# Optimization experiments

Hardware: AMD Instinct MI355X
Metric: run time of the kernel (lower is better)

The kernel has to match this reference:

```python
import jax, jax.numpy as jnp
import numpy as np

B, M, IN, HID, A = 4096, 64, 3, 128, 64
D = 50.0                       # waveguide_bound
H_CONST = 5.0
PMAX = 10.0 ** (30 / 10 - 3)   # = 1.0 (30 dBm in Watts)
C_LIGHT = 3.0e8
FC = 6.0e9
DELTA_MIN = (C_LIGHT / FC) / 2.0  # 0.025
ALPHA = 0.2                    # LeakyReLU slope


def setup_inputs() -> dict:
    key = jax.random.key(0)
    ks = jax.random.split(key, 9)
    s = lambda k, sh: (jax.random.normal(k, sh, jnp.float32) * 0.1)
    return {
        "users": jax.random.normal(ks[0], (B, M, IN), jnp.float32),
        "W1": s(ks[1], (IN, HID)),    # GAT layer 1 projection (applied as h @ W)
        "a1": s(ks[2], (2 * HID,)),   # GAT layer 1 attention vector
        "W2": s(ks[3], (HID, HID)),   # GAT layer 2 projection
        "a2": s(ks[4], (2 * HID,)),
        "mw1": s(ks[5], (HID, 32)),   # MLP Linear(hidden, 32)
        "mb1": jnp.zeros((32,), jnp.float32),
        "mw2": s(ks[6], (32, 2 * A)), # MLP Linear(32, 2*num_antennas)
        "mb2": jnp.zeros((2 * A,), jnp.float32),
    }


def gat_layer(h, W, a):
    # Wh: [B, M, d]
    Wh = h @ W
    d = W.shape[1]
    # e[b,i,j] = leakyrelu( cat(Wh_i, Wh_j) . a ) = leakyrelu( Wh_i.a[:d] + Wh_j.a[d:] )
    si = Wh @ a[:d]          # [B, M]
    sj = Wh @ a[d:]          # [B, M]
    e = jax.nn.leaky_relu(si[:, :, None] + sj[:, None, :], ALPHA)  # [B, M, M]
    attn = jax.nn.softmax(e, axis=-1)  # softmax over neighbors j (dropout p=0 -> identity)
    h_prime = jnp.einsum('bij,bjd->bid', attn, Wh)
    return jax.nn.elu(h_prime)


def reference(users, W1, a1, W2, a2, mw1, mb1, mw2, mb2):
    h = gat_layer(users, W1, a1)
    h = gat_layer(h, W2, a2)
    pooled = jnp.max(h, axis=1)                      # [B, hidden]
    readout = jax.nn.relu(pooled @ mw1 + mb1) @ mw2 + mb2  # [B, 2A]
    raw_delta, raw_power = readout[:, :A], readout[:, A:]
    eps = 1e-6
    raw_delta = jax.nn.relu(raw_delta) + eps
    raw_power = jax.nn.relu(raw_power) + eps
    Bmax = 2.0 * D - (A - 1) * DELTA_MIN
    delta = Bmax * raw_delta / (jnp.sum(raw_delta, axis=1, keepdims=True) + eps)
    power = PMAX * raw_power / (jnp.sum(raw_power, axis=1, keepdims=True) + eps)
    return power, delta
```

## Files before the change

kernel.cpp:

```cpp
#include <hip/hip_runtime.h>

#define NBATCH 4096
#define OUT2 (NBATCH * 64)

typedef _Float16 f16;
typedef __attribute__((ext_vector_type(8))) _Float16 f16x8;
typedef __attribute__((ext_vector_type(4))) float f32x4;

__device__ __forceinline__ float lrelu(float x) { return fmaxf(x, 0.2f * x); }
__device__ __forceinline__ float elu1(float x)  { return x > 0.0f ? x : __expf(x) - 1.0f; }
__device__ __forceinline__ void lds_fence() {
    asm volatile("s_waitcnt lgkmcnt(0)" ::: "memory");
}
__device__ __forceinline__ unsigned pk2(float a, float b) {
    union { f16 h[2]; unsigned u; } t;
    t.h[0] = (f16)a; t.h[1] = (f16)b;
    return t.u;
}
__device__ __forceinline__ f16x8 xpose(unsigned p0l, unsigned p0h,
                                       unsigned p1l, unsigned p1h,
                                       int s0, int s1, bool hiSel) {
    const unsigned a0l = (unsigned)__shfl((int)p0l, s0, 64);
    const unsigned a0h = (unsigned)__shfl((int)p0h, s0, 64);
    const unsigned b0l = (unsigned)__shfl((int)p0l, s1, 64);
    const unsigned b0h = (unsigned)__shfl((int)p0h, s1, 64);
    const unsigned a1l = (unsigned)__shfl((int)p1l, s0, 64);
    const unsigned a1h = (unsigned)__shfl((int)p1h, s0, 64);
    const unsigned b1l = (unsigned)__shfl((int)p1l, s1, 64);
    const unsigned b1h = (unsigned)__shfl((int)p1h, s1, 64);
    union { unsigned u[4]; f16x8 v; } o;
    o.u[0] = hiSel ? a1l : a0l;
    o.u[1] = hiSel ? a1h : a0h;
    o.u[2] = hiSel ? b1l : b0l;
    o.u[3] = hiSel ? b1h : b0h;
    return o.v;
}

__global__ void prep(const float* __restrict__ W2, const float* __restrict__ W1,
                     const float* __restrict__ a1, const float* __restrict__ a2,
                     f16* __restrict__ w2b, float* __restrict__ w1a, f16* __restrict__ w2ab) {
    const int flat = blockIdx.x * 256 + threadIdx.x;
    const int slot = flat >> 3, j = flat & 7;
    const int F2T = slot >> 8, kf = (slot >> 6) & 3, ln = slot & 63;
    const int lq = ln >> 4, lr = ln & 15;
    w2b[flat] = (f16)W2[(kf * 32 + lq * 8 + j) * 128 + F2T * 16 + lr];
    if (flat < 2048) {
        const int ks = flat >> 9, ln2 = (flat >> 3) & 63, jj = flat & 7;
        const int k = ks * 32 + ((ln2 >> 4) & 3) * 8 + jj;
        const int n = ln2 & 15;
        float v = 0.f;
        if (n < 2) {
            const float* av = a2 + n * 128;
            for (int f2 = 0; f2 < 128; ++f2) v = fmaf(W2[k * 128 + f2], av[f2], v);
        }
        w2ab[flat] = (f16)v;
    }
    if (flat >= 16381) {
        const int c = flat - 16381;
        float si = 0.f, sj = 0.f;
        for (int f = 0; f < 128; ++f) {
            const float w = W1[c * 128 + f];
            si = fmaf(w, a1[f], si);
            sj = fmaf(w, a1[128 + f], sj);
        }
        w1a[c] = si; w1a[3 + c] = sj;
    }
}

__global__ __launch_bounds__(256, 2)
void gat_kernel(const float* __restrict__ users,
                const float* __restrict__ W1,
                const f16* __restrict__ w2b,
                const float* __restrict__ w1a,
                const f16* __restrict__ w2ab,
                const float* __restrict__ mw1,
                const float* __restrict__ mb1,
                const float* __restrict__ mw2,
                const float* __restrict__ mb2,
                float* __restrict__ out)
{
    const int wid  = threadIdx.x >> 6;
    const int b    = blockIdx.x * 4 + wid;
    const int lane = threadIdx.x & 63;
    const int lr   = lane & 15;
    const int lq   = lane >> 4;
    const int s0   = (lane & 15) | ((lane & 16) << 1);
    const int s1   = s0 + 16;
    const bool hiSel = (lane & 32) != 0;

    __shared__ __align__(16) char smem[4 * 1280];
    char*  sw    = smem + wid * 1280;
    float* sSi   = (float*)(sw);
    float* sSj   = (float*)(sw + 256);
    float* sPool = (float*)(sw + 512);
    float* sHid  = (float*)(sw + 1024);

    const float* u = users + b * 192;

    {
        const float x = u[lane * 3], y = u[lane * 3 + 1], z = u[lane * 3 + 2];
        sSi[lane] = fmaf(x, w1a[0], fmaf(y, w1a[1], z * w1a[2]));
        sSj[lane] = fmaf(x, w1a[3], fmaf(y, w1a[4], z * w1a[5]));
    }
    lds_fence();

    f16x8 bfr[4];
    {
        float sjv[16];
        *(float4*)&sjv[0]  = *(const float4*)&sSj[lq * 8];
        *(float4*)&sjv[4]  = *(const float4*)&sSj[lq * 8 + 4];
        *(float4*)&sjv[8]  = *(const float4*)&sSj[32 + lq * 8];
        *(float4*)&sjv[12] = *(const float4*)&sSj[32 + lq * 8 + 4];
        f16x8 ap[4][2];
        #pragma unroll
        for (int mt = 0; mt < 4; ++mt) {
            const float si = sSi[mt * 16 + lr];
            float pv[16];
            float lsum = 0.f;
            #pragma unroll
            for (int jj = 0; jj < 8; ++jj) {
                const float p0 = __expf(lrelu(si + sjv[jj]));
                const float p1 = __expf(lrelu(si + sjv[8 + jj]));
                pv[jj] = p0; pv[8 + jj] = p1;
                lsum += p0 + p1;
            }
            lsum += __shfl_xor(lsum, 16, 64);
            lsum += __shfl_xor(lsum, 32, 64);
            const float inv = 1.0f / lsum;
            #pragma unroll
            for (int jj = 0; jj < 8; ++jj) {
                ap[mt][0][jj] = (f16)(pv[jj] * inv);
                ap[mt][1][jj] = (f16)(pv[8 + jj] * inv);
            }
        }
        f16x8 af2[2];
        #pragma unroll
        for (int ks = 0; ks < 2; ++ks) {
            #pragma unroll
            for (int jj = 0; jj < 8; ++jj) {
                const int node = ks * 32 + lq * 8 + jj;
                af2[ks][jj] = (lr < 3) ? (f16)u[node * 3 + lr] : (f16)0.f;
            }
        }
        #pragma unroll
        for (int nt = 0; nt < 4; ++nt) {
            f32x4 d1 = (f32x4){0.f, 0.f, 0.f, 0.f};
            d1 = __builtin_amdgcn_mfma_f32_16x16x32_f16(af2[0], ap[nt][0], d1, 0, 0, 0);
            d1 = __builtin_amdgcn_mfma_f32_16x16x32_f16(af2[1], ap[nt][1], d1, 0, 0, 0);
            const float c0 = __shfl(d1[0], lr, 64);
            const float c1 = __shfl(d1[1], lr, 64);
            const float c2 = __shfl(d1[2], lr, 64);
            #pragma unroll
            for (int jj = 0; jj < 8; ++jj) bfr[nt][jj] = (f16)0.f;
            if (lq == 0) {
                bfr[nt][0] = (f16)c0; bfr[nt][1] = (f16)c1; bfr[nt][2] = (f16)c2;
            }
        }
    }

    f16x8 hf[4][4];
    #pragma unroll
    for (int h = 0; h < 2; ++h) {
        #pragma unroll
        for (int ksl = 0; ksl < 2; ++ksl) {
            f32x4 acc[4][2];
            #pragma unroll
            for (int tp = 0; tp < 2; ++tp) {
                const int ftl = 2 * ksl + tp;
                f16x8 af3;
                #pragma unroll
                for (int jj = 0; jj < 8; ++jj) af3[jj] = (f16)0.f;
                if (lq == 0) {
                    #pragma unroll
                    for (int jj = 0; jj < 3; ++jj)
                        af3[jj] = (f16)W1[jj * 128 + (h * 4 + ftl) * 16 + lr];
                }
                #pragma unroll
                for (int nt = 0; nt < 4; ++nt) {
                    acc[nt][tp] = (f32x4){0.f, 0.f, 0.f, 0.f};
                    acc[nt][tp] = __builtin_amdgcn_mfma_f32_16x16x32_f16(af3, bfr[nt], acc[nt][tp], 0, 0, 0);
                }
            }
            #pragma unroll
            for (int nt = 0; nt < 4; ++nt) {
                const unsigned p0l = pk2(elu1(acc[nt][0][0]), elu1(acc[nt][0][1]));
                const unsigned p0h = pk2(elu1(acc[nt][0][2]), elu1(acc[nt][0][3]));
                const unsigned p1l = pk2(elu1(acc[nt][1][0]), elu1(acc[nt][1][1]));
                const unsigned p1h = pk2(elu1(acc[nt][1][2]), elu1(acc[nt][1][3]));
                hf[nt][h * 2 + ksl] = xpose(p0l, p0h, p1l, p1h, s0, s1, hiSel);
            }
        }
    }

    {
        f32x4 sacc[4];
        #pragma unroll
        for (int mt = 0; mt < 4; ++mt) sacc[mt] = (f32x4){0.f, 0.f, 0.f, 0.f};
        #pragma unroll
        for (int ks = 0; ks < 4; ++ks) {
            f16x8 bsw = *(const f16x8*)(w2ab + (ks * 64 + lane) * 8);
            #pragma unroll
            for (int mt = 0; mt < 4; ++mt)
                sacc[mt] = __builtin_amdgcn_mfma_f32_16x16x32_f16(hf[mt][ks], bsw, sacc[mt], 0, 0, 0);
        }
        lds_fence();
        if (lr < 2) {
            float* dst = (lr == 0) ? sSi : sSj;
            #pragma unroll
            for (int mt = 0; mt < 4; ++mt)
                #pragma unroll
                for (int r = 0; r < 4; ++r)
                    dst[mt * 16 + lq * 4 + r] = sacc[mt][r];
        }
    }
    lds_fence();

    f16x8 bp[4][2];
    {
        float sjv[16];
        *(float4*)&sjv[0]  = *(const float4*)&sSj[lq * 8];
        *(float4*)&sjv[4]  = *(const float4*)&sSj[lq * 8 + 4];
        *(float4*)&sjv[8]  = *(const float4*)&sSj[32 + lq * 8];
        *(float4*)&sjv[12] = *(const float4*)&sSj[32 + lq * 8 + 4];
        #pragma unroll
        for (int mt = 0; mt < 4; ++mt) {
            const float si = sSi[mt * 16 + lr];
            float pv[16];
            float lsum = 0.f;
            #pragma unroll
            for (int jj = 0; jj < 8; ++jj) {
                const float p0 = __expf(lrelu(si + sjv[jj]));
                const float p1 = __expf(lrelu(si + sjv[8 + jj]));
                pv[jj] = p0; pv[8 + jj] = p1;
                lsum += p0 + p1;
            }
            lsum += __shfl_xor(lsum, 16, 64);
            lsum += __shfl_xor(lsum, 32, 64);
            const float inv = 1.0f / lsum;
            #pragma unroll
            for (int jj = 0; jj < 8; ++jj) {
                bp[mt][0][jj] = (f16)(pv[jj] * inv);
                bp[mt][1][jj] = (f16)(pv[8 + jj] * inv);
            }
        }
    }

    #pragma unroll
    for (int ft = 0; ft < 8; ++ft) {
        f16x8 bw2[4];
        #pragma unroll
        for (int kf = 0; kf < 4; ++kf)
            bw2[kf] = *(const f16x8*)(w2b + ((ft * 4 + kf) * 64 + lane) * 8);
        unsigned pkq[4][2];
        #pragma unroll
        for (int nt = 0; nt < 4; ++nt) {
            f32x4 acc = (f32x4){0.f, 0.f, 0.f, 0.f};
            #pragma unroll
            for (int kf = 0; kf < 4; ++kf)
                acc = __builtin_amdgcn_mfma_f32_16x16x32_f16(hf[nt][kf], bw2[kf], acc, 0, 0, 0);
            pkq[nt][0] = pk2(acc[0], acc[1]);
            pkq[nt][1] = pk2(acc[2], acc[3]);
        }
        const f16x8 bh0 = xpose(pkq[0][0], pkq[0][1], pkq[1][0], pkq[1][1], s0, s1, hiSel);
        const f16x8 bh1 = xpose(pkq[2][0], pkq[2][1], pkq[3][0], pkq[3][1], s0, s1, hiSel);

        float mx = -1e30f;
        #pragma unroll
        for (int mt = 0; mt < 4; ++mt) {
            f32x4 acc = (f32x4){0.f, 0.f, 0.f, 0.f};
            acc = __builtin_amdgcn_mfma_f32_16x16x32_f16(bp[mt][0], bh0, acc, 0, 0, 0);
            acc = __builtin_amdgcn_mfma_f32_16x16x32_f16(bp[mt][1], bh1, acc, 0, 0, 0);
            mx = fmaxf(mx, fmaxf(fmaxf(acc[0], acc[1]), fmaxf(acc[2], acc[3])));
        }
        mx = fmaxf(mx, __shfl_xor(mx, 16, 64));
        mx = fmaxf(mx, __shfl_xor(mx, 32, 64));
        if (lane < 16) sPool[ft * 16 + lane] = elu1(mx);
    }
    lds_fence();

    {
        const int o = lane & 31, hh = lane >> 5;
        float s0r = 0.f;
        #pragma unroll 8
        for (int kk = 0; kk < 64; ++kk) {
            const int c = hh * 64 + kk;
            s0r = fmaf(sPool[c], mw1[c * 32 + o], s0r);
        }
        s0r += __shfl_xor(s0r, 32, 64);
        if (lane < 32) sHid[lane] = fmaxf(s0r + mb1[o], 0.0f);
    }
    lds_fence();
    {
        float sA = mb2[lane], sB = mb2[64 + lane];
        #pragma unroll 8
        for (int q = 0; q < 32; ++q) {
            const float wA = mw2[q * 128 + lane];
            const float wB = mw2[q * 128 + 64 + lane];
            const float h0 = sHid[q];
            sA = fmaf(h0, wA, sA);  sB = fmaf(h0, wB, sB);
        }
        float rA = fmaxf(sA, 0.0f) + 1e-6f, rB = fmaxf(sB, 0.0f) + 1e-6f;
        float uA = rA, uB = rB;
        #pragma unroll
        for (int m = 1; m < 64; m <<= 1) {
            uA += __shfl_xor(uA, m, 64);  uB += __shfl_xor(uB, m, 64);
        }
        out[b * 64 + lane]        = rB / (uB + 1e-6f);
        out[OUT2 + b * 64 + lane] = 98.425f * rA / (uA + 1e-6f);
    }
}

extern "C" void kernel_launch(void* const* d_in, const int* in_sizes, int n_in,
                              void* d_out, int out_size, void* d_ws, size_t ws_size,
                              hipStream_t stream) {
    const float* users = (const float*)d_in[0];
    const float* W1    = (const float*)d_in[1];
    const float* a1    = (const float*)d_in[2];
    const float* W2    = (const float*)d_in[3];
    const float* a2    = (const float*)d_in[4];
    const float* mw1   = (const float*)d_in[5];
    const float* mb1   = (const float*)d_in[6];
    const float* mw2   = (const float*)d_in[7];
    const float* mb2   = (const float*)d_in[8];
    float* out = (float*)d_out;

    f16*   w2b  = (f16*)d_ws;
    float* w1a  = (float*)((char*)d_ws + 32768);
    f16*   w2ab = (f16*)((char*)d_ws + 32800);

    prep<<<64, 256, 0, stream>>>(W2, W1, a1, a2, w2b, w1a, w2ab);
    gat_kernel<<<NBATCH / 4, 256, 0, stream>>>(users, W1, w2b, w1a, w2ab,
                                               mw1, mb1, mw2, mb2, out);
}
```

Before: 113.2 us.

## Stagger wave start with s_sleep, pack f16 fragments, software-pipeline W2 loads

Each wave now sleeps at launch for a number of s_sleep iterations set by its block and wave index, so that waves hit global memory and MFMA at different times. The softmax attention fragments and the layer-1 B fragments are built with packed half2 conversions instead of per-element f16 writes. The layer-2 feature-tile loop is no longer unrolled and is software-pipelined, loading the next tile's W2 fragments from global memory while the current tile's MFMAs run. The deliberate sleep adds latency to every wave, and the rolled loop may cost scheduling freedom and registers in exchange for smaller code.

```diff
diff --git a/kernel.cpp b/kernel.cpp
--- a/kernel.cpp
+++ b/kernel.cpp
@@ -17,6 +17,8 @@
     t.h[0] = (f16)a; t.h[1] = (f16)b;
     return t.u;
 }
+union F16x8U { unsigned u[4]; f16x8 v; };
+
 __device__ __forceinline__ f16x8 xpose(unsigned p0l, unsigned p0h,
                                        unsigned p1l, unsigned p1h,
                                        int s0, int s1, bool hiSel) {
@@ -28,7 +30,7 @@
     const unsigned a1h = (unsigned)__shfl((int)p1h, s0, 64);
     const unsigned b1l = (unsigned)__shfl((int)p1l, s1, 64);
     const unsigned b1h = (unsigned)__shfl((int)p1h, s1, 64);
-    union { unsigned u[4]; f16x8 v; } o;
+    F16x8U o;
     o.u[0] = hiSel ? a1l : a0l;
     o.u[1] = hiSel ? a1h : a0h;
     o.u[2] = hiSel ? b1l : b0l;
@@ -88,6 +90,11 @@
     const int s1   = s0 + 16;
     const bool hiSel = (lane & 32) != 0;
 
+    {
+        const int stg = __builtin_amdgcn_readfirstlane(((blockIdx.x >> 3) & 3) * 4 + wid);
+        for (int i = 0; i < stg; ++i) __builtin_amdgcn_s_sleep(16);
+    }
+
     __shared__ __align__(16) char smem[4 * 1280];
     char*  sw    = smem + wid * 1280;
     float* sSi   = (float*)(sw);
@@ -127,11 +134,14 @@
             lsum += __shfl_xor(lsum, 16, 64);
             lsum += __shfl_xor(lsum, 32, 64);
             const float inv = 1.0f / lsum;
-            #pragma unroll
-            for (int jj = 0; jj < 8; ++jj) {
-                ap[mt][0][jj] = (f16)(pv[jj] * inv);
-                ap[mt][1][jj] = (f16)(pv[8 + jj] * inv);
-            }
+            F16x8U a0, a1;
+            #pragma unroll
+            for (int d = 0; d < 4; ++d) {
+                a0.u[d] = pk2(pv[2 * d] * inv,     pv[2 * d + 1] * inv);
+                a1.u[d] = pk2(pv[8 + 2 * d] * inv, pv[8 + 2 * d + 1] * inv);
+            }
+            ap[mt][0] = a0.v;
+            ap[mt][1] = a1.v;
         }
         f16x8 af2[2];
         #pragma unroll
@@ -150,11 +160,11 @@
             const float c0 = __shfl(d1[0], lr, 64);
             const float c1 = __shfl(d1[1], lr, 64);
             const float c2 = __shfl(d1[2], lr, 64);
-            #pragma unroll
-            for (int jj = 0; jj < 8; ++jj) bfr[nt][jj] = (f16)0.f;
-            if (lq == 0) {
-                bfr[nt][0] = (f16)c0; bfr[nt][1] = (f16)c1; bfr[nt][2] = (f16)c2;
-            }
+            F16x8U t;
+            t.u[0] = (lq == 0) ? pk2(c0, c1)   : 0u;
+            t.u[1] = (lq == 0) ? pk2(c2, 0.0f) : 0u;
+            t.u[2] = 0u; t.u[3] = 0u;
+            bfr[nt] = t.v;
         }
     }
 
@@ -237,44 +247,62 @@
             lsum += __shfl_xor(lsum, 16, 64);
             lsum += __shfl_xor(lsum, 32, 64);
             const float inv = 1.0f / lsum;
-            #pragma unroll
-            for (int jj = 0; jj < 8; ++jj) {
-                bp[mt][0][jj] = (f16)(pv[jj] * inv);
-                bp[mt][1][jj] = (f16)(pv[8 + jj] * inv);
-            }
-        }
-    }
-
-    #pragma unroll
-    for (int ft = 0; ft < 8; ++ft) {
-        f16x8 bw2[4];
+            F16x8U b0, b1;
+            #pragma unroll
+            for (int d = 0; d < 4; ++d) {
+                b0.u[d] = pk2(pv[2 * d] * inv,     pv[2 * d + 1] * inv);
+                b1.u[d] = pk2(pv[8 + 2 * d] * inv, pv[8 + 2 * d + 1] * inv);
+            }
+            bp[mt][0] = b0.v;
+            bp[mt][1] = b1.v;
+        }
+    }
+
+    {
+        f16x8 bw2c[4];
         #pragma unroll
         for (int kf = 0; kf < 4; ++kf)
-            bw2[kf] = *(const f16x8*)(w2b + ((ft * 4 + kf) * 64 + lane) * 8);
-        unsigned pkq[4][2];
-        #pragma unroll
-        for (int nt = 0; nt < 4; ++nt) {
-            f32x4 acc = (f32x4){0.f, 0.f, 0.f, 0.f};
-            #pragma unroll
-            for (int kf = 0; kf < 4; ++kf)
-                acc = __builtin_amdgcn_mfma_f32_16x16x32_f16(hf[nt][kf], bw2[kf], acc, 0, 0, 0);
-            pkq[nt][0] = pk2(acc[0], acc[1]);
-            pkq[nt][1] = pk2(acc[2], acc[3]);
-        }
-        const f16x8 bh0 = xpose(pkq[0][0], pkq[0][1], pkq[1][0], pkq[1][1], s0, s1, hiSel);
-        const f16x8 bh1 = xpose(pkq[2][0], pkq[2][1], pkq[3][0], pkq[3][1], s0, s1, hiSel);
-
-        float mx = -1e30f;
-        #pragma unroll
-        for (int mt = 0; mt < 4; ++mt) {
-            f32x4 acc = (f32x4){0.f, 0.f, 0.f, 0.f};
-            acc = __builtin_amdgcn_mfma_f32_16x16x32_f16(bp[mt][0], bh0, acc, 0, 0, 0);
-            acc = __builtin_amdgcn_mfma_f32_16x16x32_f16(bp[mt][1], bh1, acc, 0, 0, 0);
-            mx = fmaxf(mx, fmaxf(fmaxf(acc[0], acc[1]), fmaxf(acc[2], acc[3])));
-        }
-        mx = fmaxf(mx, __shfl_xor(mx, 16, 64));
-        mx = fmaxf(mx, __shfl_xor(mx, 32, 64));
-        if (lane < 16) sPool[ft * 16 + lane] = elu1(mx);
+            bw2c[kf] = *(const f16x8*)(w2b + ((0 * 4 + kf) * 64 + lane) * 8);
+
+        #pragma unroll 1
+        for (int ft = 0; ft < 8; ++ft) {
+            f16x8 bw2n[4];
+            if (ft < 7) {
+                #pragma unroll
+                for (int kf = 0; kf < 4; ++kf)
+                    bw2n[kf] = *(const f16x8*)(w2b + (((ft + 1) * 4 + kf) * 64 + lane) * 8);
+            }
+
+            unsigned pkq[4][2];
+            #pragma unroll
+            for (int nt = 0; nt < 4; ++nt) {
+                f32x4 acc = (f32x4){0.f, 0.f, 0.f, 0.f};
+                #pragma unroll
+                for (int kf = 0; kf < 4; ++kf)
+                    acc = __builtin_amdgcn_mfma_f32_16x16x32_f16(hf[nt][kf], bw2c[kf], acc, 0, 0, 0);
+                pkq[nt][0] = pk2(acc[0], acc[1]);
+                pkq[nt][1] = pk2(acc[2], acc[3]);
+            }
+            const f16x8 bh0 = xpose(pkq[0][0], pkq[0][1], pkq[1][0], pkq[1][1], s0, s1, hiSel);
+            const f16x8 bh1 = xpose(pkq[2][0], pkq[2][1], pkq[3][0], pkq[3][1], s0, s1, hiSel);
+
+            float mx = -1e30f;
+            #pragma unroll
+            for (int mt = 0; mt < 4; ++mt) {
+                f32x4 acc = (f32x4){0.f, 0.f, 0.f, 0.f};
+                acc = __builtin_amdgcn_mfma_f32_16x16x32_f16(bp[mt][0], bh0, acc, 0, 0, 0);
+                acc = __builtin_amdgcn_mfma_f32_16x16x32_f16(bp[mt][1], bh1, acc, 0, 0, 0);
+                mx = fmaxf(mx, fmaxf(fmaxf(acc[0], acc[1]), fmaxf(acc[2], acc[3])));
+            }
+            mx = fmaxf(mx, __shfl_xor(mx, 16, 64));
+            mx = fmaxf(mx, __shfl_xor(mx, 32, 64));
+            if (lane < 16) sPool[ft * 16 + lane] = elu1(mx);
+
+            if (ft < 7) {
+                #pragma unroll
+                for (int kf = 0; kf < 4; ++kf) bw2c[kf] = bw2n[kf];
+            }
+        }
     }
     lds_fence();
 
```

New measurement: 117.4 us. 3.7% more time.
